# Performance work log

Measured on AMD Instinct MI355X. Metric: run time of the kernel, lower is better.

## Reference

```python
import jax, jax.numpy as jnp
import numpy as np

B, S, F, V, E = 4, 64, 64, 16384, 512
NUM_POS = 256  # nn.Embedding(num_embeddings=256)


def setup_inputs() -> dict:
    key = jax.random.key(0)
    k_idx, k_w, k_p, k_f = jax.random.split(key, 4)
    # the module asserts x is one-hot: build random token ids, one-hot encode
    ids = jax.random.randint(k_idx, (B, S, F), 0, V)
    x = jax.nn.one_hot(ids, V, dtype=jnp.float32)  # [B,S,F,V]
    W = jax.random.normal(k_w, (E, V), dtype=jnp.float32) * 0.02   # Linear weight [out,in]
    pos_emb = jax.random.normal(k_p, (NUM_POS, E), dtype=jnp.float32)
    fmap_emb = jax.random.normal(k_f, (NUM_POS, E), dtype=jnp.float32)
    return {"x": x, "W": W, "pos_emb": pos_emb, "fmap_emb": fmap_emb}


def reference(x, W, pos_emb, fmap_emb):
    # position_idx=None branch: out[b,s,f] = W @ x[b,s,f] + pos_emb[s] + fmap_emb[f]
    b, s, f, v = x.shape
    tok = jnp.einsum('bsfv,ev->bsfe', x, W)          # one-hot matmul == gather of W columns
    out = tok + pos_emb[:s][None, :, None, :] + fmap_emb[:f][None, None, :, :]
    return out
```

## Files before the change

kernel.cpp:

```cpp
#include <hip/hip_runtime.h>
#include <hip/hip_bf16.h>

#define BB 4
#define SS 64
#define FF 64
#define VV 16384
#define EE 512

#define TILE 32
__global__ __launch_bounds__(256) void transpose_w(const float* __restrict__ W,
                                                   float* __restrict__ Wt) {
    __shared__ float tile[TILE][TILE + 1];
    const int v0 = blockIdx.x * TILE;
    const int e0 = blockIdx.y * TILE;
    const int tx = threadIdx.x;
    const int ty = threadIdx.y;

#pragma unroll
    for (int j = 0; j < TILE; j += 8)
        tile[ty + j][tx] = W[(size_t)(e0 + ty + j) * VV + v0 + tx];
    __syncthreads();
#pragma unroll
    for (int j = 0; j < TILE; j += 8)
        Wt[(size_t)(v0 + ty + j) * EE + e0 + tx] = tile[tx][ty + j];
}

__global__ __launch_bounds__(256) void combined_embed(
        const float* __restrict__ x,
        const float* __restrict__ W,
        const float* __restrict__ Wt,
        const float* __restrict__ pos_emb,
        const float* __restrict__ fmap_emb,
        float* __restrict__ out,
        int use_wt) {
    const int lane = threadIdx.x & 63;
    const int wave = threadIdx.x >> 6;
    const int row  = blockIdx.x * 4 + wave;

    const float4* xr = (const float4*)(x + (size_t)row * VV);
    int idx = 0;
#pragma unroll 1
    for (int it = 0; it < VV / (64 * 4); ++it) {
        float4 v = xr[it * 64 + lane];
        int p = -1;
        if (v.x != 0.0f) p = 0;
        else if (v.y != 0.0f) p = 1;
        else if (v.z != 0.0f) p = 2;
        else if (v.w != 0.0f) p = 3;
        if (__any(p >= 0)) {
            int cand = (p >= 0) ? (it * 256 + lane * 4 + p) : 0x7fffffff;
#pragma unroll
            for (int off = 32; off; off >>= 1)
                cand = min(cand, __shfl_xor(cand, off));
            idx = cand;
            break;
        }
    }

    const int f = row & (FF - 1);
    const int s = (row >> 6) & (SS - 1);
    const float4* prow = (const float4*)(pos_emb  + (size_t)s * EE);
    const float4* frow = (const float4*)(fmap_emb + (size_t)f * EE);
    float4*       orow = (float4*)(out + (size_t)row * EE);

    if (use_wt) {
        const float4* wrow = (const float4*)(Wt + (size_t)idx * EE);
#pragma unroll
        for (int j = 0; j < 2; ++j) {
            const int e4 = j * 64 + lane;
            float4 w = wrow[e4];
            float4 p = prow[e4];
            float4 fm = frow[e4];
            orow[e4] = make_float4(w.x + p.x + fm.x, w.y + p.y + fm.y,
                                   w.z + p.z + fm.z, w.w + p.w + fm.w);
        }
    } else {
#pragma unroll
        for (int j = 0; j < 2; ++j) {
            const int e4 = j * 64 + lane;
            float4 p = prow[e4];
            float4 fm = frow[e4];
            float4 w;
            w.x = W[(size_t)(e4 * 4 + 0) * VV + idx];
            w.y = W[(size_t)(e4 * 4 + 1) * VV + idx];
            w.z = W[(size_t)(e4 * 4 + 2) * VV + idx];
            w.w = W[(size_t)(e4 * 4 + 3) * VV + idx];
            orow[e4] = make_float4(w.x + p.x + fm.x, w.y + p.y + fm.y,
                                   w.z + p.z + fm.z, w.w + p.w + fm.w);
        }
    }
}

extern "C" void kernel_launch(void* const* d_in, const int* in_sizes, int n_in,
                              void* d_out, int out_size, void* d_ws, size_t ws_size,
                              hipStream_t stream) {
    const float* x        = (const float*)d_in[0];
    const float* W        = (const float*)d_in[1];
    const float* pos_emb  = (const float*)d_in[2];
    const float* fmap_emb = (const float*)d_in[3];
    float* out = (float*)d_out;

    const size_t wt_bytes = (size_t)VV * EE * sizeof(float);
    const int use_wt = (ws_size >= wt_bytes) ? 1 : 0;
    float* Wt = (float*)d_ws;

    if (use_wt) {
        dim3 grid(VV / TILE, EE / TILE);
        dim3 block(32, 8);
        transpose_w<<<grid, block, 0, stream>>>(W, Wt);
    }

    const int rows = BB * SS * FF;
    combined_embed<<<rows / 4, 256, 0, stream>>>(x, W, Wt, pos_emb, fmap_emb,
                                                 out, use_wt);
}
```

Baseline: 1.304 ms.

## Split one-hot index search into a fully parallel streaming kernel before the gather

Replaces the per-wave serial early-exit scan of each one-hot row with a separate find_ids kernel. That kernel streams all of x with every thread checking four float4s and writing the hot index to a workspace array. A lightweight embed_rows kernel then gathers the transposed W row and adds the positional and fmap embeddings. The aim is to turn a latency-bound, dependent per-row scan into a bandwidth-bound coalesced stream, at the cost of reading all of x instead of stopping early. It relies on each row having exactly one nonzero; an all-zero row would leave its id unwritten. The fallback path also swaps the shuffle-min reduction for a ballot/ffs lookup.

```diff
diff --git a/kernel.cpp b/kernel.cpp
--- a/kernel.cpp
+++ b/kernel.cpp
@@ -6,6 +6,7 @@
 #define FF 64
 #define VV 16384
 #define EE 512
+#define ROWS (BB * SS * FF)
 
 #define TILE 32
 __global__ __launch_bounds__(256) void transpose_w(const float* __restrict__ W,
@@ -25,34 +26,82 @@
         Wt[(size_t)(v0 + ty + j) * EE + e0 + tx] = tile[tx][ty + j];
 }
 
-__global__ __launch_bounds__(256) void combined_embed(
-        const float* __restrict__ x,
-        const float* __restrict__ W,
+__global__ __launch_bounds__(256) void find_ids(const float* __restrict__ x,
+                                                int* __restrict__ ids) {
+    const float4* x4 = (const float4*)x;
+    const size_t base4 = (size_t)blockIdx.x * 1024;
+    int found = -1;
+#pragma unroll
+    for (int j = 0; j < 4; ++j) {
+        const size_t off = base4 + (size_t)j * 256 + threadIdx.x;
+        float4 v = x4[off];
+        int p = -1;
+        if (v.x != 0.0f) p = 0;
+        if (v.y != 0.0f) p = 1;
+        if (v.z != 0.0f) p = 2;
+        if (v.w != 0.0f) p = 3;
+        if (p >= 0) found = (int)(off << 2) + p;
+    }
+    if (found >= 0) {
+        const int row = found >> 14;
+        ids[row] = found & (VV - 1);
+    }
+}
+
+__global__ __launch_bounds__(128) void embed_rows(
+        const int* __restrict__ ids,
         const float* __restrict__ Wt,
         const float* __restrict__ pos_emb,
         const float* __restrict__ fmap_emb,
-        float* __restrict__ out,
-        int use_wt) {
+        float* __restrict__ out) {
     const int lane = threadIdx.x & 63;
     const int wave = threadIdx.x >> 6;
-    const int row  = blockIdx.x * 4 + wave;
+    const int row  = blockIdx.x * 2 + wave;
+    const int idx  = ids[row];
+
+    const int f = row & (FF - 1);
+    const int s = (row >> 6) & (SS - 1);
+    const float4* wrow = (const float4*)(Wt + (size_t)idx * EE);
+    const float4* prow = (const float4*)(pos_emb  + (size_t)s * EE);
+    const float4* frow = (const float4*)(fmap_emb + (size_t)f * EE);
+    float4*       orow = (float4*)(out + (size_t)row * EE);
+
+#pragma unroll
+    for (int j = 0; j < 2; ++j) {
+        const int e4 = j * 64 + lane;
+        float4 w = wrow[e4];
+        float4 p = prow[e4];
+        float4 fm = frow[e4];
+        orow[e4] = make_float4(w.x + p.x + fm.x, w.y + p.y + fm.y,
+                               w.z + p.z + fm.z, w.w + p.w + fm.w);
+    }
+}
+
+__global__ __launch_bounds__(128) void combined_fallback(
+        const float* __restrict__ x,
+        const float* __restrict__ W,
+        const float* __restrict__ pos_emb,
+        const float* __restrict__ fmap_emb,
+        float* __restrict__ out) {
+    const int lane = threadIdx.x & 63;
+    const int wave = threadIdx.x >> 6;
+    const int row  = blockIdx.x * 2 + wave;
 
     const float4* xr = (const float4*)(x + (size_t)row * VV);
     int idx = 0;
 #pragma unroll 1
-    for (int it = 0; it < VV / (64 * 4); ++it) {
+    for (int it = 0; it < VV / 256; ++it) {
         float4 v = xr[it * 64 + lane];
         int p = -1;
         if (v.x != 0.0f) p = 0;
-        else if (v.y != 0.0f) p = 1;
-        else if (v.z != 0.0f) p = 2;
-        else if (v.w != 0.0f) p = 3;
-        if (__any(p >= 0)) {
-            int cand = (p >= 0) ? (it * 256 + lane * 4 + p) : 0x7fffffff;
-#pragma unroll
-            for (int off = 32; off; off >>= 1)
-                cand = min(cand, __shfl_xor(cand, off));
-            idx = cand;
+        if (v.y != 0.0f) p = 1;
+        if (v.z != 0.0f) p = 2;
+        if (v.w != 0.0f) p = 3;
+        unsigned long long m = __ballot(p >= 0);
+        if (m) {
+            const int src = (int)__ffsll(m) - 1;
+            const int pl  = __shfl(p, src);
+            idx = it * 256 + src * 4 + pl;
             break;
         }
     }
@@ -62,32 +111,18 @@
     const float4* prow = (const float4*)(pos_emb  + (size_t)s * EE);
     const float4* frow = (const float4*)(fmap_emb + (size_t)f * EE);
     float4*       orow = (float4*)(out + (size_t)row * EE);
-
-    if (use_wt) {
-        const float4* wrow = (const float4*)(Wt + (size_t)idx * EE);
 #pragma unroll
-        for (int j = 0; j < 2; ++j) {
-            const int e4 = j * 64 + lane;
-            float4 w = wrow[e4];
-            float4 p = prow[e4];
-            float4 fm = frow[e4];
-            orow[e4] = make_float4(w.x + p.x + fm.x, w.y + p.y + fm.y,
-                                   w.z + p.z + fm.z, w.w + p.w + fm.w);
-        }
-    } else {
-#pragma unroll
-        for (int j = 0; j < 2; ++j) {
-            const int e4 = j * 64 + lane;
-            float4 p = prow[e4];
-            float4 fm = frow[e4];
-            float4 w;
-            w.x = W[(size_t)(e4 * 4 + 0) * VV + idx];
-            w.y = W[(size_t)(e4 * 4 + 1) * VV + idx];
-            w.z = W[(size_t)(e4 * 4 + 2) * VV + idx];
-            w.w = W[(size_t)(e4 * 4 + 3) * VV + idx];
-            orow[e4] = make_float4(w.x + p.x + fm.x, w.y + p.y + fm.y,
-                                   w.z + p.z + fm.z, w.w + p.w + fm.w);
-        }
+    for (int j = 0; j < 2; ++j) {
+        const int e4 = j * 64 + lane;
+        float4 p = prow[e4];
+        float4 fm = frow[e4];
+        float4 w;
+        w.x = W[(size_t)(e4 * 4 + 0) * VV + idx];
+        w.y = W[(size_t)(e4 * 4 + 1) * VV + idx];
+        w.z = W[(size_t)(e4 * 4 + 2) * VV + idx];
+        w.w = W[(size_t)(e4 * 4 + 3) * VV + idx];
+        orow[e4] = make_float4(w.x + p.x + fm.x, w.y + p.y + fm.y,
+                               w.z + p.z + fm.z, w.w + p.w + fm.w);
     }
 }
 
@@ -100,17 +135,22 @@
     const float* fmap_emb = (const float*)d_in[3];
     float* out = (float*)d_out;
 
-    const size_t wt_bytes = (size_t)VV * EE * sizeof(float);
-    const int use_wt = (ws_size >= wt_bytes) ? 1 : 0;
-    float* Wt = (float*)d_ws;
+    const size_t wt_bytes  = (size_t)VV * EE * sizeof(float);
+    const size_t ids_bytes = (size_t)ROWS * sizeof(int);
 
-    if (use_wt) {
-        dim3 grid(VV / TILE, EE / TILE);
-        dim3 block(32, 8);
-        transpose_w<<<grid, block, 0, stream>>>(W, Wt);
+    if (ws_size >= wt_bytes + ids_bytes) {
+        float* Wt  = (float*)d_ws;
+        int*   ids = (int*)((char*)d_ws + wt_bytes);
+
+        dim3 tgrid(VV / TILE, EE / TILE);
+        dim3 tblock(32, 8);
+        transpose_w<<<tgrid, tblock, 0, stream>>>(W, Wt);
+
+        const int nblocks = (BB * SS * FF * VV) / 4096;
+        find_ids<<<nblocks, 256, 0, stream>>>(x, ids);
+
+        embed_rows<<<ROWS / 2, 128, 0, stream>>>(ids, Wt, pos_emb, fmap_emb, out);
+    } else {
+        combined_fallback<<<ROWS / 2, 128, 0, stream>>>(x, W, pos_emb, fmap_emb, out);
     }
-
-    const int rows = BB * SS * FF;
-    combined_embed<<<rows / 4, 256, 0, stream>>>(x, W, Wt, pos_emb, fmap_emb,
-                                                 out, use_wt);
 }
```

After: 1.347 ms. +3.3%, slower.
